# Performance work log

Measured on AMD Instinct MI355X. Metric: run time of the kernel, lower is better.

## Reference

```python
import jax, jax.numpy as jnp
import numpy as np

D = 512      # embeddings_dim (in_features == out_features)
H = 4        # num_heads
MID = 2048   # mid_features
B, S = 4, 2048
EPS = 1e-5


def _ln(x, g, b):
    mu = jnp.mean(x, axis=-1, keepdims=True)
    var = jnp.mean(jnp.square(x - mu), axis=-1, keepdims=True)
    return g * (x - mu) / jnp.sqrt(var + EPS) + b


def setup_inputs() -> dict:
    key = jax.random.key(0)
    ks = jax.random.split(key, 16)
    w = 0.02  # weight init scale
    return {
        "x_encoder": jax.random.normal(ks[0], (B, S, D), jnp.float32),
        "x_decoder": jax.random.normal(ks[1], (B, S, D), jnp.float32),
        # per-head full-width projections (each head is a D->D Linear)
        "Wq": jax.random.normal(ks[2], (H, D, D), jnp.float32) * w,
        "bq": jnp.zeros((H, D), jnp.float32),
        "Wk": jax.random.normal(ks[3], (H, D, D), jnp.float32) * w,
        "bk": jnp.zeros((H, D), jnp.float32),
        "Wv": jax.random.normal(ks[4], (H, D, D), jnp.float32) * w,
        "bv": jnp.zeros((H, D), jnp.float32),
        # out_reshaper: Rearrange('b h s d -> b s (d h)') then Linear(D*H -> D)
        "Wo": jax.random.normal(ks[5], (D * H, D), jnp.float32) * w,
        "bo": jnp.zeros((D,), jnp.float32),
        "ln1_g": jnp.ones((D,), jnp.float32), "ln1_b": jnp.zeros((D,), jnp.float32),
        "ln2_g": jnp.ones((D,), jnp.float32), "ln2_b": jnp.zeros((D,), jnp.float32),
        # FouriFeedForward: D -> MID -> D with SELU
        "W1": jax.random.normal(ks[6], (D, MID), jnp.float32) * w,
        "b1": jnp.zeros((MID,), jnp.float32),
        "W2": jax.random.normal(ks[7], (MID, D), jnp.float32) * w,
        "b2": jnp.zeros((D,), jnp.float32),
        "ln3_g": jnp.ones((D,), jnp.float32), "ln3_b": jnp.zeros((D,), jnp.float32),
    }


def reference(x_encoder, x_decoder, Wq, bq, Wk, bk, Wv, bv, Wo, bo,
              ln1_g, ln1_b, ln2_g, ln2_b, W1, b1, W2, b2, ln3_g, ln3_b):
    # Fourier token mixing: per-batch fftn over (seq, feature) dims, keep real part
    xf = jnp.fft.fftn(x_decoder, axes=(1, 2)).real
    xd = _ln(x_decoder + xf, ln1_g, ln1_b)  # [B,S,D]

    # Linear multi-head attention: q from decoder, k/v from encoder.
    # qs/ks/vs: [B,H,S,D]; softmax over the HEAD axis (dim=1 in torch)
    qs = jax.nn.softmax(jnp.einsum('bsd,hde->bhse', xd, Wq) + bq[None, :, None, :], axis=1)
    ks = jax.nn.softmax(jnp.einsum('bsd,hde->bhse', x_encoder, Wk) + bk[None, :, None, :], axis=1)
    vs = jnp.einsum('bsd,hde->bhse', x_encoder, Wv) + bv[None, :, None, :]

    gc = jnp.einsum('bhsd,bhse->bhde', ks, vs)       # [B,H,D,D] global contexts
    out = jnp.einsum('bhsd,bhde->bhse', qs, gc)      # [B,H,S,D]

    # Rearrange 'b h s d -> b s (d h)': d is the slow axis, h the fast axis
    b, h, s, d = out.shape
    out = out.transpose(0, 2, 3, 1).reshape(b, s, d * h)
    attn = out @ Wo + bo                              # [B,S,D]

    x = _ln(xd + attn, ln2_g, ln2_b)
    ff = jax.nn.selu(x @ W1 + b1) @ W2 + b2           # dropout_p=0 (eval)
    x = _ln(x + ff, ln3_g, ln3_b)
    return x
```

## Files before the change

### kernel.cpp

```cpp
#include <hip/hip_runtime.h>
#include <stdint.h>

typedef __bf16 bf16;
typedef __bf16 bf16x8 __attribute__((ext_vector_type(8)));
typedef float f32x4 __attribute__((ext_vector_type(4)));

static __device__ __forceinline__ void async16(const void* g, void* l) {
  __builtin_amdgcn_global_load_lds(
      (__attribute__((address_space(1))) void*)g,
      (__attribute__((address_space(3))) void*)l, 16, 0, 0);
}

__global__ void __launch_bounds__(256) prep_all(
    const float* __restrict__ xdec, const float* __restrict__ xenc,
    bf16* __restrict__ Ttrig, bf16* __restrict__ Atrig2,
    bf16* __restrict__ xdec_b, bf16* __restrict__ xenc_b,
    const float* __restrict__ Wq, const float* __restrict__ Wk,
    const float* __restrict__ Wv, const float* __restrict__ Wo,
    const float* __restrict__ W1, const float* __restrict__ W2,
    bf16* __restrict__ BtQ, bf16* __restrict__ BtK, bf16* __restrict__ BtV,
    bf16* __restrict__ WoTh, bf16* __restrict__ W1T, bf16* __restrict__ W2T) {
  __shared__ bf16 tile[32][33];
  int id = blockIdx.x;
  if (id < 2048) {
    int idx = id * 256 + threadIdx.x;
    int d = idx & 511, jp = idx >> 9;
    int jj = jp >> 1, p = jp & 1;
    int t = (d * jj) & 511;
    float ang = (float)t * (6.283185307179586f / 512.0f);
    Ttrig[idx] = (bf16)(p ? __sinf(ang) : __cosf(ang));
  } else if (id < 11840) {
    int idx = (id - 2048) * 256 + threadIdx.x;
    int k = idx % 1088;
    int rr = idx / 1088;
    int r = rr % 1152, half = rr / 1152;
    float v = 0.0f;
    int tt = (r * k) & 2047;
    float ang = (float)tt * (6.283185307179586f / 2048.0f);
    if (half == 0) { if (r <= 1024 && k <= 1024) v = __cosf(ang); }
    else           { if (r <= 1023 && k >= 1 && k <= 1023) v = -__sinf(ang); }
    Atrig2[idx] = (bf16)v;
  } else if (id < 28224) {
    int i = (id - 11840) * 256 + threadIdx.x;
    xdec_b[i] = (bf16)xdec[i];
  } else if (id < 44608) {
    int i = (id - 28224) * 256 + threadIdx.x;
    xenc_b[i] = (bf16)xenc[i];
  } else {
    int id2 = id - 44608;
    int kind = id2 >> 10, t = id2 & 1023;
    const float* in; bf16* out; int R, C, rt, ct;
    bool iperm = false, qperm = false, hsel = false; int hh = 0;
    if (kind == 0)      { in = Wq; out = BtQ; R = 2048; C = 512; rt = t >> 4; ct = t & 15; iperm = true; qperm = true; }
    else if (kind == 1) { in = Wk; out = BtK; R = 2048; C = 512; rt = t >> 4; ct = t & 15; iperm = true; }
    else if (kind == 2) { in = Wv; out = BtV; R = 2048; C = 512; rt = t >> 4; ct = t & 15; iperm = true; }
    else if (kind == 3) {
      int zz = t >> 8, tt = t & 255;
      in = Wo; out = WoTh + (long)zz * 262144;
      R = 512; C = 512; rt = tt >> 4; ct = tt & 15; hsel = true; hh = zz;
    }
    else if (kind == 4) { in = W1; out = W1T; R = 512; C = 2048; rt = t >> 6; ct = t & 63; }
    else                { in = W2; out = W2T; R = 2048; C = 512; rt = t >> 4; ct = t & 15; }
    int c0 = ct * 32, r0 = rt * 32;
    int tx = threadIdx.x & 31, ty = threadIdx.x >> 5;
#pragma unroll
    for (int i = 0; i < 32; i += 8) {
      int r = r0 + ty + i;
      int rr = hsel ? (4 * r + hh) : r;
      tile[ty + i][tx] = (bf16)in[(long)rr * C + (c0 + tx)];
    }
    __syncthreads();
#pragma unroll
    for (int i = 0; i < 32; i += 8) {
      int cc = c0 + ty + i, rr = r0 + tx;
      if (iperm) {
        int e = cc, h = rr >> 9;
        int n = qperm ? ((e & 15) | (h << 4) | ((e >> 4) << 6)) : (4 * e + h);
        out[((long)n << 9) + (rr & 511)] = tile[tx][ty + i];
      } else {
        out[(long)cc * R + rr] = tile[tx][ty + i];
      }
    }
  }
}

__global__ void __launch_bounds__(256) fold_y(const bf16* __restrict__ Yt,
                                              bf16* __restrict__ Yf2) {
  int idx = blockIdx.x * 256 + threadIdx.x;
  int k = idx % 1088;
  int rr = idx / 1088;
  int j = rr & 511, z = rr >> 9;
  int b = z & 3, half = z >> 2;
  const bf16* yin = Yt + (long)b * 2097152 + (long)j * 4096;
  float v = 0.0f;
  if (half == 0) {
    if (k == 0) v = (float)yin[0];
    else if (k == 1024) v = (float)yin[1024];
    else if (k < 1024) v = (float)yin[k] + (float)yin[2048 - k];
  } else {
    if (k >= 1 && k <= 1023) v = (float)yin[2048 + k] - (float)yin[4096 - k];
  }
  Yf2[(long)z * 557056 + (long)j * 1088 + k] = (bf16)v;
}

__global__ void __launch_bounds__(256) ln1_kernel(
    const float* __restrict__ xdec, const bf16* __restrict__ CSb,
    const float* __restrict__ g, const float* __restrict__ be,
    bf16* __restrict__ outb) {
  const int row = blockIdx.x, t = threadIdx.x;
  const int b = row >> 11, s = row & 2047;
  const int sp = (s <= 1024) ? s : 2048 - s;
  const float sgn = (s <= 1024) ? 1.0f : -1.0f;
  const bf16* Crow = CSb + ((long)b * 1152 + sp) * 512;
  const bf16* Srow = CSb + ((long)(b + 4) * 1152 + sp) * 512;
  const long base = (long)row * 512;
  float v0 = xdec[base + t] + (float)Crow[t] + sgn * (float)Srow[t];
  float v1 = xdec[base + t + 256] + (float)Crow[t + 256] + sgn * (float)Srow[t + 256];
  float sm = v0 + v1, q = v0 * v0 + v1 * v1;
#pragma unroll
  for (int off = 32; off > 0; off >>= 1) {
    sm += __shfl_down(sm, off);
    q += __shfl_down(q, off);
  }
  __shared__ float red[8];
  const int wv = t >> 6, ln = t & 63;
  if (ln == 0) { red[wv] = sm; red[wv + 4] = q; }
  __syncthreads();
  float S = red[0] + red[1] + red[2] + red[3];
  float Q = red[4] + red[5] + red[6] + red[7];
  float mu = S * (1.0f / 512.0f);
  float var = Q * (1.0f / 512.0f) - mu * mu;
  float rstd = rsqrtf(var + 1e-5f);
  outb[base + t] = (bf16)(g[t] * (v0 - mu) * rstd + be[t]);
  outb[base + t + 256] = (bf16)(g[t + 256] * (v1 - mu) * rstd + be[t + 256]);
}

__global__ void __launch_bounds__(256) softmax_kv(
    const bf16* __restrict__ klog, bf16* __restrict__ ksT,
    const bf16* __restrict__ vlog, bf16* __restrict__ vsT) {
  __shared__ bf16 lds[4 * 64 * 64];
  const int bid = blockIdx.x, t = threadIdx.x;
  const bool isK = bid < 1024;
  int tb = isK ? bid : (bid - 1024);
  const bf16* src = isK ? klog : vlog;
  bf16* dst = isK ? ksT : vsT;
  int b = tb >> 8, rem = tb & 255;
  int s0 = (rem >> 3) << 6, e0 = (rem & 7) << 6;
  int te = t & 63, tr = t >> 6;
#pragma unroll
  for (int i = 0; i < 16; ++i) {
    int s = tr + (i << 2);
    bf16 raw[4] __attribute__((aligned(8)));
    *(uint2*)raw = *(const uint2*)(src + ((long)(b * 2048 + s0 + s) * 2048 + 4 * (e0 + te)));
    float x0 = (float)raw[0], x1 = (float)raw[1], x2 = (float)raw[2], x3 = (float)raw[3];
    if (isK) {
      float m = fmaxf(fmaxf(x0, x1), fmaxf(x2, x3));
      float y0 = __expf(x0 - m), y1 = __expf(x1 - m), y2 = __expf(x2 - m), y3 = __expf(x3 - m);
      float rs = 1.0f / (y0 + y1 + y2 + y3);
      x0 = y0 * rs; x1 = y1 * rs; x2 = y2 * rs; x3 = y3 * rs;
    }
    int cp = ((((s >> 2) ^ (te & 15)) << 2) | (s & 3));
    int base = te * 64 + cp;
    lds[base] = (bf16)x0;
    lds[4096 + base] = (bf16)x1;
    lds[8192 + base] = (bf16)x2;
    lds[12288 + base] = (bf16)x3;
  }
  __syncthreads();
  int sc = t & 15, r = t >> 4;
#pragma unroll
  for (int i = 0; i < 16; ++i) {
    int he = r + (i << 4);
    int h = he >> 6, e = he & 63;
    int cp = (sc ^ (e & 15)) << 2;
    bf16 tmp[4] __attribute__((aligned(8)));
    *(uint2*)tmp = *(const uint2*)&lds[h * 4096 + e * 64 + cp];
    *(uint2*)(dst + ((long)(b * 4 + h) * 512 + e0 + e) * 2048 + s0 + (sc << 2)) =
        *(const uint2*)tmp;
  }
}

template <typename TA, typename TB, int WRITE_BF16, int WRITE_F32>
__global__ void __launch_bounds__(256) ln_kernel(
    const TA* __restrict__ A, const TB* __restrict__ Bv,
    const float* __restrict__ g, const float* __restrict__ be,
    bf16* __restrict__ outb, float* __restrict__ outf) {
  const int row = blockIdx.x, t = threadIdx.x;
  const long base = (long)row * 512;
  float v0 = (float)A[base + t] + (float)Bv[base + t];
  float v1 = (float)A[base + t + 256] + (float)Bv[base + t + 256];
  float s = v0 + v1, q = v0 * v0 + v1 * v1;
#pragma unroll
  for (int off = 32; off > 0; off >>= 1) {
    s += __shfl_down(s, off);
    q += __shfl_down(q, off);
  }
  __shared__ float red[8];
  const int wv = t >> 6, ln = t & 63;
  if (ln == 0) { red[wv] = s; red[wv + 4] = q; }
  __syncthreads();
  float S = red[0] + red[1] + red[2] + red[3];
  float Q = red[4] + red[5] + red[6] + red[7];
  float mu = S * (1.0f / 512.0f);
  float var = Q * (1.0f / 512.0f) - mu * mu;
  float rstd = rsqrtf(var + 1e-5f);
  float o0 = g[t] * (v0 - mu) * rstd + be[t];
  float o1 = g[t + 256] * (v1 - mu) * rstd + be[t + 256];
  if (WRITE_BF16) { outb[base + t] = (bf16)o0; outb[base + t + 256] = (bf16)o1; }
  if (WRITE_F32)  { outf[base + t] = o0; outf[base + t + 256] = o1; }
}

template <int BN, int ADDR_MODE, int HAS_BIAS, int DO_SELU, int F32OUT, int SWIZ,
          int AHEAD = 0>
__global__ void __launch_bounds__(256, 2) gemm_bt(
    const bf16* __restrict__ A, const bf16* __restrict__ Bt,
    const float* __restrict__ bias, void* __restrict__ Cout,
    int N, int K, long sAz, long sBz, long sBiasz, long sCz,
    int gx, int gy, int gin) {
  __shared__ __align__(16) bf16 lA[128 * 64];
  __shared__ __align__(16) bf16 lB[BN * 64];
  int x, y, z;
  {
    int id = blockIdx.x;
    if (SWIZ == 0) {
      x = id % gx; int t2 = id / gx; y = t2 % gy; z = t2 / gy;
    } else {
      int xcd = id & 7, r = id >> 3;
      int inner = r % gin, G = xcd + 8 * (r / gin);
      if (SWIZ == 1)      { y = G; x = inner % gx; z = inner / gx; }
      else if (SWIZ == 2) { z = G; x = inner % gx; y = inner / gx; }
      else                { x = G; y = inner % gy; z = inner / gy; }
    }
  }
  A  += (AHEAD == 1) ? sAz * (z & 3) : (AHEAD == 2) ? sAz * (z >> 2) : sAz * z;
  Bt += sBz * z;
  const int m0 = y * 128, n0 = x * BN;
  const int t = threadIdx.x;
  const int lane = t & 63, wave = t >> 6;
  const int srow = t >> 3;
  const int pch  = t & 7;
  const int lch  = pch ^ (srow & 7);
  const bf16* Ag = A  + (long)(m0 + srow) * K + lch * 8;
  const bf16* Bg = Bt + (long)(n0 + srow) * K + lch * 8;
  bf16* lAp = lA + srow * 64 + pch * 8;
  bf16* lBp = lB + srow * 64 + pch * 8;
  constexpr int MI = (BN == 128) ? 4 : 2;
  const int wm = (BN == 128) ? (wave >> 1) * 64 : wave * 32;
  const int wn = (BN == 128) ? (wave & 1) * 64 : 0;
  const int fr = lane & 15, fq = lane >> 4;

  f32x4 acc[MI][4] = {};

  for (int k0 = 0; k0 < K; k0 += 64) {
    __syncthreads();
#pragma unroll
    for (int i = 0; i < 4; ++i)
      async16(Ag + k0 + (long)(32 * i) * K, lAp + 32 * i * 64);
#pragma unroll
    for (int i = 0; i < BN / 32; ++i)
      async16(Bg + k0 + (long)(32 * i) * K, lBp + 32 * i * 64);
    __syncthreads();
#pragma unroll
    for (int kk = 0; kk < 2; ++kk) {
      bf16x8 av[MI], bfrag[4];
#pragma unroll
      for (int mi = 0; mi < MI; ++mi) {
        int r = wm + mi * 16 + fr;
        int c = (kk * 4 + fq) ^ (r & 7);
        av[mi] = *(const bf16x8*)&lA[r * 64 + c * 8];
      }
#pragma unroll
      for (int ni = 0; ni < 4; ++ni) {
        int r = wn + ni * 16 + fr;
        int c = (kk * 4 + fq) ^ (r & 7);
        bfrag[ni] = *(const bf16x8*)&lB[r * 64 + c * 8];
      }
#pragma unroll
      for (int mi = 0; mi < MI; ++mi)
#pragma unroll
        for (int ni = 0; ni < 4; ++ni)
          acc[mi][ni] = __builtin_amdgcn_mfma_f32_16x16x32_bf16(
              av[mi], bfrag[ni], acc[mi][ni], 0, 0, 0);
    }
  }

#pragma unroll
  for (int mi = 0; mi < MI; ++mi) {
#pragma unroll
    for (int ni = 0; ni < 4; ++ni) {
      const int col = n0 + wn + ni * 16 + fr;
      float bias_v = 0.0f;
      if (HAS_BIAS == 1) bias_v = bias[sBiasz * z + col];
      if (ADDR_MODE == 7) {
        const int b = z >> 2, h = z & 3;
#pragma unroll
        for (int r = 0; r < 4; ++r) {
          const int row = m0 + wm + mi * 16 + fq * 4 + r;
          ((bf16*)Cout)[((long)(b * 512 + row)) * 2048 + h * 512 + col] =
              (bf16)(acc[mi][ni][r] + bias_v);
        }
      } else if (ADDR_MODE == 9) {
        const int b = z >> 2, h = z & 3;
        const int kidx = (col & 15) | (h << 4) | ((col >> 4) << 6);
#pragma unroll
        for (int r = 0; r < 4; ++r) {
          const int row = m0 + wm + mi * 16 + fq * 4 + r;
          ((bf16*)Cout)[((long)(b * 512 + row)) * 2048 + kidx] =
              (bf16)(acc[mi][ni][r] + bias_v);
        }
      } else {
#pragma unroll
        for (int r = 0; r < 4; ++r) {
          const int row = m0 + wm + mi * 16 + fq * 4 + r;
          float v = acc[mi][ni][r] + bias_v;
          if (DO_SELU) v = v > 0.0f ? 1.0507009873554805f * v
                                    : 1.7580993408473766f * (__expf(v) - 1.0f);
          long addr = sCz * z + (long)row * N + col;
          if (F32OUT) ((float*)Cout)[addr] = v;
          else        ((bf16*)Cout)[addr] = (bf16)v;
        }
      }
    }
  }
}

__global__ void __launch_bounds__(256, 2) gemm_qkv(
    const bf16* __restrict__ Aq, const bf16* __restrict__ Aenc,
    const bf16* __restrict__ BQ, const bf16* __restrict__ BK,
    const bf16* __restrict__ BV,
    const float* __restrict__ bq, const float* __restrict__ bk,
    const float* __restrict__ bv,
    bf16* __restrict__ qs2, bf16* __restrict__ klog, bf16* __restrict__ vlog) {
  __shared__ __align__(16) bf16 lA[128 * 64];
  __shared__ __align__(16) bf16 lB[128 * 64];
  const int id = blockIdx.x;
  const int seg = id >> 10, sid = id & 1023;
  const int xcd = sid & 7, r = sid >> 3;
  const int x = r & 15, y = xcd + 8 * (r >> 4);
  const bf16 *A, *Bt; bf16* out; const float* bias;
  if (seg == 0)      { A = Aq;   Bt = BQ; out = qs2;  bias = bq; }
  else if (seg == 1) { A = Aenc; Bt = BK; out = klog; bias = bk; }
  else               { A = Aenc; Bt = BV; out = vlog; bias = bv; }
  const int K = 512;
  const int m0 = y * 128, n0 = x * 128;
  const int t = threadIdx.x;
  const int lane = t & 63, wave = t >> 6;
  const int srow = t >> 3, pch = t & 7, lch = pch ^ (srow & 7);
  const bf16* Ag = A  + (long)(m0 + srow) * K + lch * 8;
  const bf16* Bg = Bt + (long)(n0 + srow) * K + lch * 8;
  bf16* lAp = lA + srow * 64 + pch * 8;
  bf16* lBp = lB + srow * 64 + pch * 8;
  const int wm = (wave >> 1) * 64, wn = (wave & 1) * 64;
  const int fr = lane & 15, fq = lane >> 4;

  f32x4 acc[4][4] = {};
  for (int k0 = 0; k0 < K; k0 += 64) {
    __syncthreads();
#pragma unroll
    for (int i = 0; i < 4; ++i) {
      async16(Ag + k0 + (long)(32 * i) * K, lAp + 32 * i * 64);
      async16(Bg + k0 + (long)(32 * i) * K, lBp + 32 * i * 64);
    }
    __syncthreads();
#pragma unroll
    for (int kk = 0; kk < 2; ++kk) {
      bf16x8 av[4], bfrag[4];
#pragma unroll
      for (int mi = 0; mi < 4; ++mi) {
        int rr = wm + mi * 16 + fr;
        int c = (kk * 4 + fq) ^ (rr & 7);
        av[mi] = *(const bf16x8*)&lA[rr * 64 + c * 8];
      }
#pragma unroll
      for (int ni = 0; ni < 4; ++ni) {
        int rr = wn + ni * 16 + fr;
        int c = (kk * 4 + fq) ^ (rr & 7);
        bfrag[ni] = *(const bf16x8*)&lB[rr * 64 + c * 8];
      }
#pragma unroll
      for (int mi = 0; mi < 4; ++mi)
#pragma unroll
        for (int ni = 0; ni < 4; ++ni)
          acc[mi][ni] = __builtin_amdgcn_mfma_f32_16x16x32_bf16(
              av[mi], bfrag[ni], acc[mi][ni], 0, 0, 0);
    }
  }

  if (seg == 0) {
    const int ebase = fr + 16 * ((n0 + wn) >> 6);
    const float b0 = bias[ebase], b1 = bias[512 + ebase],
                b2 = bias[1024 + ebase], b3 = bias[1536 + ebase];
#pragma unroll
    for (int mi = 0; mi < 4; ++mi) {
#pragma unroll
      for (int r = 0; r < 4; ++r) {
        const int row = m0 + wm + mi * 16 + fq * 4 + r;
        float v0 = acc[mi][0][r] + b0;
        float v1 = acc[mi][1][r] + b1;
        float v2 = acc[mi][2][r] + b2;
        float v3 = acc[mi][3][r] + b3;
        float m = fmaxf(fmaxf(v0, v1), fmaxf(v2, v3));
        float p0 = __expf(v0 - m), p1 = __expf(v1 - m),
              p2 = __expf(v2 - m), p3 = __expf(v3 - m);
        float rs = 1.0f / (p0 + p1 + p2 + p3);
        const long ob = (long)row * 2048 + n0 + wn + fr;
        out[ob]      = (bf16)(p0 * rs);
        out[ob + 16] = (bf16)(p1 * rs);
        out[ob + 32] = (bf16)(p2 * rs);
        out[ob + 48] = (bf16)(p3 * rs);
      }
    }
  } else {
#pragma unroll
    for (int mi = 0; mi < 4; ++mi) {
#pragma unroll
      for (int ni = 0; ni < 4; ++ni) {
        const int col = n0 + wn + ni * 16 + fr;
        const float bias_v = bias[(col & 3) * 512 + (col >> 2)];
#pragma unroll
        for (int r = 0; r < 4; ++r) {
          const int row = m0 + wm + mi * 16 + fq * 4 + r;
          out[(long)row * 2048 + col] = (bf16)(acc[mi][ni][r] + bias_v);
        }
      }
    }
  }
}

extern "C" void kernel_launch(void* const* d_in, const int* in_sizes, int n_in,
                              void* d_out, int out_size, void* d_ws, size_t ws_size,
                              hipStream_t stream) {
  (void)in_sizes; (void)n_in; (void)out_size; (void)ws_size;
  const float* x_enc = (const float*)d_in[0];
  const float* x_dec = (const float*)d_in[1];
  const float* Wq = (const float*)d_in[2];
  const float* bq = (const float*)d_in[3];
  const float* Wk = (const float*)d_in[4];
  const float* bk = (const float*)d_in[5];
  const float* Wv = (const float*)d_in[6];
  const float* bv = (const float*)d_in[7];
  const float* Wo = (const float*)d_in[8];
  const float* bo = (const float*)d_in[9];
  const float* g1 = (const float*)d_in[10];
  const float* be1 = (const float*)d_in[11];
  const float* g2 = (const float*)d_in[12];
  const float* be2 = (const float*)d_in[13];
  const float* W1 = (const float*)d_in[14];
  const float* b1 = (const float*)d_in[15];
  const float* W2 = (const float*)d_in[16];
  const float* b2 = (const float*)d_in[17];
  const float* g3 = (const float*)d_in[18];
  const float* be3 = (const float*)d_in[19];

  char* ws = (char*)d_ws;
  const size_t MB = 1u << 20;
  bf16*  midb   = (bf16*) (ws + 0);
  bf16*  klog   = (bf16*) (ws + 32 * MB);
  bf16*  attn_b = (bf16*) (ws + 32 * MB);
  bf16*  vlog   = (bf16*) (ws + 64 * MB);
  bf16*  gc     = (bf16*) (ws + 64 * MB);
  bf16*  ff_b   = (bf16*) (ws + 72 * MB);
  bf16*  Atrig2 = (bf16*) (ws + 96 * MB);
  bf16*  Ttrig  = (bf16*) (ws + 101 * MB);
  bf16*  CSb    = (bf16*) (ws + 102 * MB);
  bf16*  qs2    = (bf16*) (ws + 96 * MB);
  bf16*  xenc_b = (bf16*) (ws + 128 * MB);
  bf16*  BtQ    = (bf16*) (ws + 136 * MB);
  bf16*  BtK    = (bf16*) (ws + 138 * MB);
  bf16*  BtV    = (bf16*) (ws + 140 * MB);
  bf16*  ksT    = (bf16*) (ws + 128 * MB);
  bf16*  vsT    = (bf16*) (ws + 160 * MB);
  bf16*  xd_b   = (bf16*) (ws + 192 * MB);
  bf16*  x2_b   = (bf16*) (ws + 200 * MB);
  bf16*  gwT    = (bf16*) (ws + 208 * MB);
  bf16*  Yt     = (bf16*) (ws + 216 * MB);
  bf16*  Yf2    = (bf16*) (ws + 232 * MB);
  bf16*  WoTh   = (bf16*) (ws + 241 * MB);
  bf16*  W1T    = (bf16*) (ws + 243 * MB);
  bf16*  W2T    = (bf16*) (ws + 245 * MB);
  bf16*  xdec_b = (bf16*) (ws + 247 * MB);

  prep_all<<<50752, 256, 0, stream>>>(x_dec, x_enc, Ttrig, Atrig2, xdec_b, xenc_b,
                                      Wq, Wk, Wv, Wo, W1, W2,
                                      BtQ, BtK, BtV, WoTh, W1T, W2T);

  gemm_bt<128, 0, 0, 0, 0, 3><<<512, 256, 0, stream>>>(
      Ttrig, xdec_b, nullptr, Yt, 2048, 512, 0L, 1048576L, 0L, 2097152L, 16, 8, 32);
  fold_y<<<17408, 256, 0, stream>>>(Yt, Yf2);
  gemm_bt<64, 0, 0, 0, 0, 2, 2><<<576, 256, 0, stream>>>(
      Atrig2, Yf2, nullptr, CSb, 512, 1088, 1253376L, 557056L, 0L, 589824L, 8, 9, 72);
  ln1_kernel<<<8192, 256, 0, stream>>>(x_dec, CSb, g1, be1, xd_b);

  gemm_qkv<<<3072, 256, 0, stream>>>(xd_b, xenc_b, BtQ, BtK, BtV,
                                     bq, bk, bv, qs2, klog, vlog);
  softmax_kv<<<2048, 256, 0, stream>>>(klog, ksT, vlog, vsT);
  gemm_bt<64, 0, 0, 0, 0, 2><<<512, 256, 0, stream>>>(
      ksT, vsT, nullptr, gc, 512, 2048, 1048576L, 1048576L, 0L, 262144L, 8, 4, 32);
  gemm_bt<64, 9, 0, 0, 0, 2, 1><<<512, 256, 0, stream>>>(
      WoTh, gc, nullptr, gwT, 512, 512, 262144L, 262144L, 0L, 0L, 8, 4, 32);
  gemm_bt<64, 0, 1, 0, 0, 1><<<512, 256, 0, stream>>>(
      qs2, gwT, bo, attn_b, 512, 2048, 4194304L, 1048576L, 0L, 1048576L, 8, 16, 32);
  ln_kernel<bf16, bf16, 1, 0><<<8192, 256, 0, stream>>>(
      xd_b, attn_b, g2, be2, x2_b, nullptr);

  gemm_bt<128, 0, 1, 1, 0, 1><<<1024, 256, 0, stream>>>(
      x2_b, W1T, b1, midb, 2048, 512, 0L, 0L, 0L, 0L, 16, 64, 16);
  gemm_bt<64, 0, 1, 0, 0, 1><<<512, 256, 0, stream>>>(
      midb, W2T, b2, ff_b, 512, 2048, 0L, 0L, 0L, 0L, 8, 64, 8);
  ln_kernel<bf16, bf16, 0, 1><<<8192, 256, 0, stream>>>(
      x2_b, ff_b, g3, be3, nullptr, (float*)d_out);
}
```

Before: 406.9 us.

## Horizontally fuse independent Fourier GEMMs with KV, softmax and Q/context kernels

Refactors the GEMM, QKV and softmax kernels into inlineable device bodies and builds three combined kernels. Each one dispatches independent work by block index: the K/V projection with the Fourier Yt GEMM, the K/V softmax with the Fourier CS GEMM, and the Q projection with the global-context GEMM. The goal is to fill the GPU better when individual grids are small, to cut tail effects, and to remove kernel launches. The Q projection moves after LN1 and BtQ moves to a different workspace slot. In exchange, the combined kernels share one LDS size and one launch bound, which may raise register pressure or lower occupancy for the lighter parts.

After: 410.7 us. Within noise of the previous version (+0.9%).

```diff
diff --git a/kernel.cpp b/kernel.cpp
--- a/kernel.cpp
+++ b/kernel.cpp
@@ -135,11 +135,11 @@
   outb[base + t + 256] = (bf16)(g[t + 256] * (v1 - mu) * rstd + be[t + 256]);
 }
 
-__global__ void __launch_bounds__(256) softmax_kv(
+static __device__ __forceinline__ void smkv_body(
+    int bid, bf16* lds,
     const bf16* __restrict__ klog, bf16* __restrict__ ksT,
     const bf16* __restrict__ vlog, bf16* __restrict__ vsT) {
-  __shared__ bf16 lds[4 * 64 * 64];
-  const int bid = blockIdx.x, t = threadIdx.x;
+  const int t = threadIdx.x;
   const bool isK = bid < 1024;
   int tb = isK ? bid : (bid - 1024);
   const bf16* src = isK ? klog : vlog;
@@ -211,17 +211,15 @@
 }
 
 template <int BN, int ADDR_MODE, int HAS_BIAS, int DO_SELU, int F32OUT, int SWIZ,
-          int AHEAD = 0>
-__global__ void __launch_bounds__(256, 2) gemm_bt(
+          int AHEAD>
+static __device__ __forceinline__ void gemm_bt_body(
+    int id, bf16* lA, bf16* lB,
     const bf16* __restrict__ A, const bf16* __restrict__ Bt,
     const float* __restrict__ bias, void* __restrict__ Cout,
     int N, int K, long sAz, long sBz, long sBiasz, long sCz,
     int gx, int gy, int gin) {
-  __shared__ __align__(16) bf16 lA[128 * 64];
-  __shared__ __align__(16) bf16 lB[BN * 64];
   int x, y, z;
   {
-    int id = blockIdx.x;
     if (SWIZ == 0) {
       x = id % gx; int t2 = id / gx; y = t2 % gy; z = t2 / gy;
     } else {
@@ -324,16 +322,27 @@
   }
 }
 
-__global__ void __launch_bounds__(256, 2) gemm_qkv(
+template <int BN, int ADDR_MODE, int HAS_BIAS, int DO_SELU, int F32OUT, int SWIZ,
+          int AHEAD = 0>
+__global__ void __launch_bounds__(256, 2) gemm_bt(
+    const bf16* __restrict__ A, const bf16* __restrict__ Bt,
+    const float* __restrict__ bias, void* __restrict__ Cout,
+    int N, int K, long sAz, long sBz, long sBiasz, long sCz,
+    int gx, int gy, int gin) {
+  __shared__ __align__(16) bf16 lA[128 * 64];
+  __shared__ __align__(16) bf16 lB[BN * 64];
+  gemm_bt_body<BN, ADDR_MODE, HAS_BIAS, DO_SELU, F32OUT, SWIZ, AHEAD>(
+      blockIdx.x, lA, lB, A, Bt, bias, Cout, N, K, sAz, sBz, sBiasz, sCz, gx, gy, gin);
+}
+
+static __device__ __forceinline__ void qkv_body(
+    int id, bf16* lA, bf16* lB,
     const bf16* __restrict__ Aq, const bf16* __restrict__ Aenc,
     const bf16* __restrict__ BQ, const bf16* __restrict__ BK,
     const bf16* __restrict__ BV,
     const float* __restrict__ bq, const float* __restrict__ bk,
     const float* __restrict__ bv,
     bf16* __restrict__ qs2, bf16* __restrict__ klog, bf16* __restrict__ vlog) {
-  __shared__ __align__(16) bf16 lA[128 * 64];
-  __shared__ __align__(16) bf16 lB[128 * 64];
-  const int id = blockIdx.x;
   const int seg = id >> 10, sid = id & 1023;
   const int xcd = sid & 7, r = sid >> 3;
   const int x = r & 15, y = xcd + 8 * (r >> 4);
@@ -425,6 +434,52 @@
       }
     }
   }
+}
+
+__global__ void __launch_bounds__(256, 2) fused_kv_yt(
+    const bf16* __restrict__ Aenc, const bf16* __restrict__ BK,
+    const bf16* __restrict__ BV,
+    const float* __restrict__ bk, const float* __restrict__ bv,
+    bf16* __restrict__ klog, bf16* __restrict__ vlog,
+    const bf16* __restrict__ Ttrig, const bf16* __restrict__ xdec_b,
+    bf16* __restrict__ Yt) {
+  __shared__ __align__(16) bf16 smem[16384];
+  int id = blockIdx.x;
+  if (id < 2048)
+    qkv_body(id + 1024, smem, smem + 8192, nullptr, Aenc, nullptr, BK, BV,
+             nullptr, bk, bv, nullptr, klog, vlog);
+  else
+    gemm_bt_body<128, 0, 0, 0, 0, 3, 0>(id - 2048, smem, smem + 8192,
+        Ttrig, xdec_b, nullptr, Yt, 2048, 512, 0L, 1048576L, 0L, 2097152L, 16, 8, 32);
+}
+
+__global__ void __launch_bounds__(256, 2) fused_cs_smkv(
+    const bf16* __restrict__ klog, bf16* __restrict__ ksT,
+    const bf16* __restrict__ vlog, bf16* __restrict__ vsT,
+    const bf16* __restrict__ Atrig2, const bf16* __restrict__ Yf2,
+    bf16* __restrict__ CSb) {
+  __shared__ __align__(16) bf16 smem[16384];
+  int id = blockIdx.x;
+  if (id < 2048)
+    smkv_body(id, smem, klog, ksT, vlog, vsT);
+  else
+    gemm_bt_body<64, 0, 0, 0, 0, 2, 2>(id - 2048, smem, smem + 8192,
+        Atrig2, Yf2, nullptr, CSb, 512, 1088, 1253376L, 557056L, 0L, 589824L, 8, 9, 72);
+}
+
+__global__ void __launch_bounds__(256, 2) fused_q_gc(
+    const bf16* __restrict__ Aq, const bf16* __restrict__ BQ,
+    const float* __restrict__ bq, bf16* __restrict__ qs2,
+    const bf16* __restrict__ ksT, const bf16* __restrict__ vsT,
+    bf16* __restrict__ gc) {
+  __shared__ __align__(16) bf16 smem[16384];
+  int id = blockIdx.x;
+  if (id < 1024)
+    qkv_body(id, smem, smem + 8192, Aq, nullptr, BQ, nullptr, nullptr,
+             bq, nullptr, nullptr, qs2, nullptr, nullptr);
+  else
+    gemm_bt_body<64, 0, 0, 0, 0, 2, 0>(id - 1024, smem, smem + 8192,
+        ksT, vsT, nullptr, gc, 512, 2048, 1048576L, 1048576L, 0L, 262144L, 8, 4, 32);
 }
 
 extern "C" void kernel_launch(void* const* d_in, const int* in_sizes, int n_in,
@@ -454,6 +509,7 @@
 
   char* ws = (char*)d_ws;
   const size_t MB = 1u << 20;
+  bf16*  BtQ    = (bf16*) (ws + 0);
   bf16*  midb   = (bf16*) (ws + 0);
   bf16*  klog   = (bf16*) (ws + 32 * MB);
   bf16*  attn_b = (bf16*) (ws + 32 * MB);
@@ -465,9 +521,8 @@
   bf16*  CSb    = (bf16*) (ws + 102 * MB);
   bf16*  qs2    = (bf16*) (ws + 96 * MB);
   bf16*  xenc_b = (bf16*) (ws + 128 * MB);
-  bf16*  BtQ    = (bf16*) (ws + 136 * MB);
-  bf16*  BtK    = (bf16*) (ws + 138 * MB);
-  bf16*  BtV    = (bf16*) (ws + 140 * MB);
+  bf16*  BtK    = (bf16*) (ws + 136 * MB);
+  bf16*  BtV    = (bf16*) (ws + 138 * MB);
   bf16*  ksT    = (bf16*) (ws + 128 * MB);
   bf16*  vsT    = (bf16*) (ws + 160 * MB);
   bf16*  xd_b   = (bf16*) (ws + 192 * MB);
@@ -484,18 +539,17 @@
                                       Wq, Wk, Wv, Wo, W1, W2,
                                       BtQ, BtK, BtV, WoTh, W1T, W2T);
 
-  gemm_bt<128, 0, 0, 0, 0, 3><<<512, 256, 0, stream>>>(
-      Ttrig, xdec_b, nullptr, Yt, 2048, 512, 0L, 1048576L, 0L, 2097152L, 16, 8, 32);
+  fused_kv_yt<<<2560, 256, 0, stream>>>(xenc_b, BtK, BtV, bk, bv, klog, vlog,
+                                        Ttrig, xdec_b, Yt);
+
   fold_y<<<17408, 256, 0, stream>>>(Yt, Yf2);
-  gemm_bt<64, 0, 0, 0, 0, 2, 2><<<576, 256, 0, stream>>>(
-      Atrig2, Yf2, nullptr, CSb, 512, 1088, 1253376L, 557056L, 0L, 589824L, 8, 9, 72);
+
+  fused_cs_smkv<<<2624, 256, 0, stream>>>(klog, ksT, vlog, vsT, Atrig2, Yf2, CSb);
+
   ln1_kernel<<<8192, 256, 0, stream>>>(x_dec, CSb, g1, be1, xd_b);
 
-  gemm_qkv<<<3072, 256, 0, stream>>>(xd_b, xenc_b, BtQ, BtK, BtV,
-                                     bq, bk, bv, qs2, klog, vlog);
-  softmax_kv<<<2048, 256, 0, stream>>>(klog, ksT, vlog, vsT);
-  gemm_bt<64, 0, 0, 0, 0, 2><<<512, 256, 0, stream>>>(
-      ksT, vsT, nullptr, gc, 512, 2048, 1048576L, 1048576L, 0L, 262144L, 8, 4, 32);
+  fused_q_gc<<<1536, 256, 0, stream>>>(xd_b, BtQ, bq, qs2, ksT, vsT, gc);
+
   gemm_bt<64, 9, 0, 0, 0, 2, 1><<<512, 256, 0, stream>>>(
       WoTh, gc, nullptr, gwT, 512, 512, 262144L, 262144L, 0L, 0L, 8, 4, 32);
   gemm_bt<64, 0, 1, 0, 0, 1><<<512, 256, 0, stream>>>(
```
